# Performance work log

Hardware: AMD Instinct MI355X
Metric: run time of the kernel (lower is better)

Reference implementation:

```python
import jax, jax.numpy as jnp
import numpy as np

N = 50000          # nodes
E = 1_000_000      # edges
NODE_DIM = 16
EMB = 64           # embed_dim
OUT = 64           # out_dim per head
EA_DIM = 8         # raw edge_attr_dim
HEADS = 8
SLOPE = 0.01       # leaky_relu default negative slope
LN_EPS = 1e-5


def mlp(x, w, b, g, beta):
    # MLP(in, out): Linear -> LayerNorm -> ReLU (standard block in this repo)
    y = x @ w + b
    mu = jnp.mean(y, axis=-1, keepdims=True)
    var = jnp.var(y, axis=-1, keepdims=True)
    y = (y - mu) / jnp.sqrt(var + LN_EPS) * g + beta
    return jax.nn.relu(y)


def gat_layer(x, ea, src, tgt, W, a):
    """AA_GATlayer forward (dropout = identity at eval).
    x: [N, in], ea: [E, EMB], W: [in, OUT], a: [2*OUT + EMB]."""
    h = x @ W                                  # [N, OUT]
    d = h.shape[1]
    a_src, a_tgt, a_edge = a[:d], a[d:2 * d], a[2 * d:]
    # score = leaky_relu(a @ concat([h_src, h_tgt, ea])) without materializing the concat
    s = jax.nn.leaky_relu(h[src] @ a_src + h[tgt] @ a_tgt + ea @ a_edge, SLOPE)  # [E]
    s = s - jnp.max(s)
    e = jnp.exp(s)
    denom = jax.ops.segment_sum(e, src, num_segments=N)          # [N]
    attn = e / (denom[src] + 1e-16)                              # [E]
    h_prime = jax.ops.segment_sum(h[tgt] * attn[:, None], src, num_segments=N)  # [N, OUT]
    return jax.nn.elu(h_prime)


def setup_inputs() -> dict:
    key = jax.random.key(0)
    ks = jax.random.split(key, 16)
    sc = lambda fan_in: 1.0 / np.sqrt(fan_in)
    inp = {}
    inp["X"] = jax.random.normal(ks[0], (N, NODE_DIM), jnp.float32)
    inp["edge_attr"] = jax.random.normal(ks[1], (E, EA_DIM), jnp.float32)
    inp["edge_index"] = jax.random.randint(ks[2], (2, E), 0, N, jnp.int64)
    inp["matched_car_infra_nodes"] = jax.random.randint(ks[3], (1000,), 0, N, jnp.int64)
    # node_embed MLP params
    inp["w_node"] = jax.random.uniform(ks[4], (NODE_DIM, EMB), jnp.float32, -sc(NODE_DIM), sc(NODE_DIM))
    inp["b_node"] = jnp.zeros((EMB,), jnp.float32)
    inp["g_node"] = jnp.ones((EMB,), jnp.float32)
    inp["beta_node"] = jnp.zeros((EMB,), jnp.float32)
    # edge_attr_embed MLP params
    inp["w_edge"] = jax.random.uniform(ks[5], (EA_DIM, EMB), jnp.float32, -sc(EA_DIM), sc(EA_DIM))
    inp["b_edge"] = jnp.zeros((EMB,), jnp.float32)
    inp["g_edge"] = jnp.ones((EMB,), jnp.float32)
    inp["beta_edge"] = jnp.zeros((EMB,), jnp.float32)
    # 8 GAT heads: W [EMB,OUT], a [2*OUT+EMB]
    inp["gat_W"] = jax.random.uniform(ks[6], (HEADS, EMB, OUT), jnp.float32, -sc(EMB), sc(EMB))
    inp["gat_a"] = jax.random.uniform(ks[7], (HEADS, 2 * OUT + EMB), jnp.float32, -sc(2 * OUT + EMB), sc(2 * OUT + EMB))
    # output GAT layer: W [OUT*HEADS, OUT], a [2*OUT+EMB]
    inp["out_W"] = jax.random.uniform(ks[8], (OUT * HEADS, OUT), jnp.float32, -sc(OUT * HEADS), sc(OUT * HEADS))
    inp["out_a"] = jax.random.uniform(ks[9], (2 * OUT + EMB,), jnp.float32, -sc(2 * OUT + EMB), sc(2 * OUT + EMB))
    return inp


def reference(X, edge_attr, w_node, b_node, g_node, beta_node,
              w_edge, b_edge, g_edge, beta_edge,
              gat_W, gat_a, out_W, out_a,
              edge_index, matched_car_infra_nodes):
    src, tgt = edge_index[0], edge_index[1]
    x = mlp(X, w_node, b_node, g_node, beta_node)                  # [N, EMB]
    ea = mlp(edge_attr, w_edge, b_edge, g_edge, beta_edge)         # [E, EMB]
    heads = [gat_layer(x, ea, src, tgt, gat_W[i], gat_a[i]) for i in range(HEADS)]
    xh = jax.nn.elu(jnp.concatenate(heads, axis=1))                # [N, OUT*HEADS]
    out = gat_layer(xh, ea, src, tgt, out_W, out_a)                # [N, OUT]
    return jax.nn.log_softmax(out, axis=1)
```

## Files before the change

### kernel.cpp

```cpp
#include <hip/hip_runtime.h>
#include <hip/hip_fp16.h>

#define NN 50000
#define EE 1000000
#define HALF 25000

__device__ __forceinline__ float wsum(float v){
#pragma unroll
  for(int m=1;m<64;m<<=1) v += __shfl_xor(v,m,64);
  return v;
}
__device__ __forceinline__ unsigned encf(float f){
  unsigned u = __float_as_uint(f);
  return (u & 0x80000000u) ? ~u : (u | 0x80000000u);
}
__device__ __forceinline__ float decf(unsigned u){
  u = (u & 0x80000000u) ? (u & 0x7fffffffu) : ~u;
  return __uint_as_float(u);
}

__global__ __launch_bounds__(256) void zero_k(int* counts, int* cursor, unsigned* mx){
  int i = blockIdx.x*blockDim.x + threadIdx.x;
  if(i < NN){ counts[i] = 0; cursor[i] = 0; }
  if(i < 64) mx[i] = 0u;
}

__global__ __launch_bounds__(64) void cvec_k(const float* __restrict__ gat_W, const float* __restrict__ gat_a,
                                             float* __restrict__ cdir){
  int h = blockIdx.x, k = threadIdx.x;
  const float* W = gat_W + (size_t)h*64*64;
  const float* a = gat_a + (size_t)h*192;
  float cs = 0.f, ct = 0.f;
#pragma unroll
  for(int j=0;j<64;j++){ float wv = W[k*64+j]; cs += wv*a[j]; ct += wv*a[64+j]; }
  cdir[h*64 + k]       = cs;
  cdir[512 + h*64 + k] = ct;
}

__global__ __launch_bounds__(256) void node_mlp(const float* __restrict__ X, const float* __restrict__ w,
                                                const float* __restrict__ b, const float* __restrict__ g,
                                                const float* __restrict__ beta, const float* __restrict__ cdir,
                                                __half* __restrict__ x, float* __restrict__ ps8,
                                                float* __restrict__ pt8){
  int wid  = (blockIdx.x*blockDim.x + threadIdx.x) >> 6;
  int lane = threadIdx.x & 63;
  if(wid >= NN) return;
  float acc = b[lane];
#pragma unroll
  for(int k=0;k<16;k++) acc += X[wid*16+k] * w[k*64+lane];
  float mu  = wsum(acc) * (1.0f/64.0f);
  float d   = acc - mu;
  float var = wsum(d*d) * (1.0f/64.0f);
  float y   = d * rsqrtf(var + 1e-5f) * g[lane] + beta[lane];
  float xv  = fmaxf(y, 0.0f);
  x[(size_t)wid*64 + lane] = __float2half(xv);
#pragma unroll 1
  for(int h=0;h<8;h++){
    float a = wsum(xv * cdir[h*64+lane]);
    float c = wsum(xv * cdir[512 + h*64+lane]);
    if(lane == 0){ ps8[wid*8+h] = a; pt8[wid*8+h] = c; }
  }
}

__global__ __launch_bounds__(256) void hist_k(const int* __restrict__ src, int* __restrict__ counts){
  int e = blockIdx.x*blockDim.x + threadIdx.x;
  if(e < EE){
    int s = src[e];
    if((unsigned)s >= NN) s = 0;
    atomicAdd(&counts[s], 1);
  }
}

__global__ __launch_bounds__(256) void scan1_k(const int* __restrict__ counts, int* __restrict__ bsum){
  int i = blockIdx.x*256 + threadIdx.x;
  int v = (i < NN) ? counts[i] : 0;
  int s = v;
#pragma unroll
  for(int m=1;m<64;m<<=1) s += __shfl_xor(s,m,64);
  __shared__ int sm[4];
  if((threadIdx.x & 63) == 0) sm[threadIdx.x>>6] = s;
  __syncthreads();
  if(threadIdx.x == 0) bsum[blockIdx.x] = sm[0]+sm[1]+sm[2]+sm[3];
}

__global__ __launch_bounds__(256) void scan2_k(const int* __restrict__ bsum, int* __restrict__ bpre,
                                               int* __restrict__ offs){
  const int NB = (NN + 255)/256;
  int t = threadIdx.x;
  __shared__ int sm[256];
  int v = (t < NB) ? bsum[t] : 0;
  sm[t] = v; __syncthreads();
  for(int off=1; off<256; off<<=1){
    int u = (t >= off) ? sm[t-off] : 0;
    __syncthreads();
    sm[t] += u;
    __syncthreads();
  }
  if(t < NB) bpre[t] = sm[t] - v;
  if(t == 0) offs[NN] = EE;
}

__global__ __launch_bounds__(256) void scan3_k(const int* __restrict__ counts, const int* __restrict__ bpre,
                                               int* __restrict__ offs){
  int i = blockIdx.x*256 + threadIdx.x;
  int t = threadIdx.x;
  __shared__ int sm[256];
  int v = (i < NN) ? counts[i] : 0;
  sm[t] = v; __syncthreads();
  for(int off=1; off<256; off<<=1){
    int u = (t >= off) ? sm[t-off] : 0;
    __syncthreads();
    sm[t] += u;
    __syncthreads();
  }
  if(i < NN) offs[i] = bpre[blockIdx.x] + sm[t] - v;
}

__global__ __launch_bounds__(256) void scatter_k(const int* __restrict__ src, const int* __restrict__ tgt,
                                                 const int* __restrict__ offs, int* __restrict__ cursor,
                                                 int* __restrict__ rank, int* __restrict__ tgt_s,
                                                 int* __restrict__ src_s){
  int e = blockIdx.x*blockDim.x + threadIdx.x;
  if(e < EE){
    int s = src[e];
    if((unsigned)s >= NN) s = 0;
    int pos = offs[s] + atomicAdd(&cursor[s], 1);
    rank[e] = pos;
    int t = tgt[e];
    if((unsigned)t >= NN) t = 0;
    tgt_s[pos] = t;
    src_s[pos] = s;
  }
}

__global__ __launch_bounds__(256) void edge_mlp_q(const int* __restrict__ rank, const float* __restrict__ ea,
                                                  const float* __restrict__ w, const float* __restrict__ b,
                                                  const float* __restrict__ g, const float* __restrict__ beta,
                                                  const float* __restrict__ gat_a, const float* __restrict__ out_a,
                                                  float* __restrict__ q8, float* __restrict__ q_out){
  __shared__ float wle[512];
  __shared__ float ble[64], gle[64], bbe[64];
  __shared__ float ale[64*12];
  int tid = threadIdx.x;
  for(int idx=tid; idx<512; idx+=256){ int j=idx>>3, k=idx&7; wle[idx] = w[k*64+j]; }
  if(tid < 64){
    ble[tid] = b[tid]; gle[tid] = g[tid]; bbe[tid] = beta[tid];
#pragma unroll
    for(int r=0;r<8;r++) ale[tid*12+r] = gat_a[r*192 + 128 + tid];
    ale[tid*12+8] = out_a[128 + tid];
  }
  __syncthreads();
  int e = blockIdx.x*blockDim.x + tid;
  if(e >= EE) return;
  float4 ia = ((const float4*)ea)[(size_t)e*2];
  float4 ib = ((const float4*)ea)[(size_t)e*2+1];
  float y[64];
#pragma unroll
  for(int j=0;j<64;j++){
    float4 w0 = *(const float4*)&wle[j*8];
    float4 w1 = *(const float4*)&wle[j*8+4];
    float acc = ble[j];
    acc = fmaf(ia.x,w0.x, fmaf(ia.y,w0.y, fmaf(ia.z,w0.z, fmaf(ia.w,w0.w, acc))));
    acc = fmaf(ib.x,w1.x, fmaf(ib.y,w1.y, fmaf(ib.z,w1.z, fmaf(ib.w,w1.w, acc))));
    y[j] = acc;
  }
  float mu = 0.f;
#pragma unroll
  for(int j=0;j<64;j++) mu += y[j];
  mu *= (1.0f/64.0f);
  float var = 0.f;
#pragma unroll
  for(int j=0;j<64;j++){ float d = y[j]-mu; var += d*d; }
  var *= (1.0f/64.0f);
  float inv = rsqrtf(var + 1e-5f);
#pragma unroll
  for(int j=0;j<64;j++) y[j] = fmaxf((y[j]-mu)*inv*gle[j] + bbe[j], 0.0f);
  float qv[9];
#pragma unroll
  for(int r=0;r<9;r++) qv[r] = 0.f;
#pragma unroll
  for(int j=0;j<64;j++){
    float4 a0 = *(const float4*)&ale[j*12];
    float4 a1 = *(const float4*)&ale[j*12+4];
    float a8  = ale[j*12+8];
    float yj = y[j];
    qv[0]=fmaf(yj,a0.x,qv[0]); qv[1]=fmaf(yj,a0.y,qv[1]); qv[2]=fmaf(yj,a0.z,qv[2]); qv[3]=fmaf(yj,a0.w,qv[3]);
    qv[4]=fmaf(yj,a1.x,qv[4]); qv[5]=fmaf(yj,a1.y,qv[5]); qv[6]=fmaf(yj,a1.z,qv[6]); qv[7]=fmaf(yj,a1.w,qv[7]);
    qv[8]=fmaf(yj,a8 ,qv[8]);
  }
  int r = rank[e];
  ((float4*)q8)[(size_t)r*2]   = make_float4(qv[0],qv[1],qv[2],qv[3]);
  ((float4*)q8)[(size_t)r*2+1] = make_float4(qv[4],qv[5],qv[6],qv[7]);
  q_out[r] = qv[8];
}

__global__ __launch_bounds__(256) void maxq_k(const float* __restrict__ q8, const float* __restrict__ q_out,
                                              unsigned* __restrict__ mx){
  float m[9];
#pragma unroll
  for(int r=0;r<9;r++) m[r] = -3.0e38f;
  for(int i = blockIdx.x*256 + threadIdx.x; i < EE; i += gridDim.x*256){
    float4 a = ((const float4*)q8)[(size_t)i*2];
    float4 c = ((const float4*)q8)[(size_t)i*2+1];
    m[0]=fmaxf(m[0],a.x); m[1]=fmaxf(m[1],a.y); m[2]=fmaxf(m[2],a.z); m[3]=fmaxf(m[3],a.w);
    m[4]=fmaxf(m[4],c.x); m[5]=fmaxf(m[5],c.y); m[6]=fmaxf(m[6],c.z); m[7]=fmaxf(m[7],c.w);
    m[8]=fmaxf(m[8], q_out[i]);
  }
#pragma unroll
  for(int r=0;r<9;r++)
#pragma unroll
    for(int msk=1;msk<64;msk<<=1) m[r] = fmaxf(m[r], __shfl_xor(m[r],msk,64));
  __shared__ float sm[4][9];
  int wv = threadIdx.x>>6, lane = threadIdx.x&63;
  if(lane == 0){
#pragma unroll
    for(int r=0;r<9;r++) sm[wv][r] = m[r];
  }
  __syncthreads();
  if(threadIdx.x < 9){
    int r = threadIdx.x;
    float v = fmaxf(fmaxf(sm[0][r],sm[1][r]), fmaxf(sm[2][r],sm[3][r]));
    atomicMax(&mx[r], encf(v));
  }
}

__global__ __launch_bounds__(256) void maxp_k(const float* __restrict__ ps8, const float* __restrict__ pt8,
                                              unsigned* __restrict__ mx){
  float m[16];
#pragma unroll
  for(int r=0;r<16;r++) m[r] = -3.0e38f;
  for(int i = blockIdx.x*256 + threadIdx.x; i < NN; i += gridDim.x*256){
    float4 a = ((const float4*)ps8)[(size_t)i*2];
    float4 c = ((const float4*)ps8)[(size_t)i*2+1];
    float4 d = ((const float4*)pt8)[(size_t)i*2];
    float4 e = ((const float4*)pt8)[(size_t)i*2+1];
    m[0]=fmaxf(m[0],a.x); m[1]=fmaxf(m[1],a.y); m[2]=fmaxf(m[2],a.z); m[3]=fmaxf(m[3],a.w);
    m[4]=fmaxf(m[4],c.x); m[5]=fmaxf(m[5],c.y); m[6]=fmaxf(m[6],c.z); m[7]=fmaxf(m[7],c.w);
    m[8]=fmaxf(m[8],d.x); m[9]=fmaxf(m[9],d.y); m[10]=fmaxf(m[10],d.z); m[11]=fmaxf(m[11],d.w);
    m[12]=fmaxf(m[12],e.x); m[13]=fmaxf(m[13],e.y); m[14]=fmaxf(m[14],e.z); m[15]=fmaxf(m[15],e.w);
  }
#pragma unroll
  for(int r=0;r<16;r++)
#pragma unroll
    for(int msk=1;msk<64;msk<<=1) m[r] = fmaxf(m[r], __shfl_xor(m[r],msk,64));
  __shared__ float sm[4][16];
  int wv = threadIdx.x>>6, lane = threadIdx.x&63;
  if(lane == 0){
#pragma unroll
    for(int r=0;r<16;r++) sm[wv][r] = m[r];
  }
  __syncthreads();
  if(threadIdx.x < 16){
    int r = threadIdx.x;
    float v = fmaxf(fmaxf(sm[0][r],sm[1][r]), fmaxf(sm[2][r],sm[3][r]));
    atomicMax(&mx[16+r], encf(v));
  }
}

__global__ __launch_bounds__(256) void maxpo_k(const float* __restrict__ ps_o, const float* __restrict__ pt_o,
                                               unsigned* __restrict__ mx){
  float m0 = -3.0e38f, m1 = -3.0e38f;
  for(int i = blockIdx.x*256 + threadIdx.x; i < NN; i += gridDim.x*256){
    m0 = fmaxf(m0, ps_o[i]); m1 = fmaxf(m1, pt_o[i]);
  }
#pragma unroll
  for(int msk=1;msk<64;msk<<=1){ m0=fmaxf(m0,__shfl_xor(m0,msk,64)); m1=fmaxf(m1,__shfl_xor(m1,msk,64)); }
  __shared__ float sm[4][2];
  int wv = threadIdx.x>>6, lane = threadIdx.x&63;
  if(lane == 0){ sm[wv][0]=m0; sm[wv][1]=m1; }
  __syncthreads();
  if(threadIdx.x < 2){
    int r = threadIdx.x;
    float v = fmaxf(fmaxf(sm[0][r],sm[1][r]), fmaxf(sm[2][r],sm[3][r]));
    atomicMax(&mx[32+r], encf(v));
  }
}

__global__ __launch_bounds__(256) void score_k(const int* __restrict__ src_s, const int* __restrict__ tgt_s,
                                               const float* __restrict__ ps8, const float* __restrict__ pt8,
                                               const unsigned* __restrict__ mx, const float* __restrict__ q8,
                                               __half* __restrict__ w8h){
  int i = blockIdx.x*256 + threadIdx.x;
  if(i >= EE) return;
  int s = src_s[i], t = tgt_s[i];
  float4 qa = ((const float4*)q8)[(size_t)i*2];
  float4 qb = ((const float4*)q8)[(size_t)i*2+1];
  float4 sa = ((const float4*)ps8)[(size_t)s*2];
  float4 sb = ((const float4*)ps8)[(size_t)s*2+1];
  float4 ta = ((const float4*)pt8)[(size_t)t*2];
  float4 tb = ((const float4*)pt8)[(size_t)t*2+1];
  float sv[8] = {qa.x+sa.x+ta.x, qa.y+sa.y+ta.y, qa.z+sa.z+ta.z, qa.w+sa.w+ta.w,
                 qb.x+sb.x+tb.x, qb.y+sb.y+tb.y, qb.z+sb.z+tb.z, qb.w+sb.w+tb.w};
  float wv[8];
#pragma unroll
  for(int h=0;h<8;h++){
    float B = decf(mx[h]) + decf(mx[16+h]) + decf(mx[24+h]);
    float M = (B > 0.f) ? B : 0.01f*B;
    float x = sv[h];
    x = (x > 0.f) ? x : 0.01f*x;
    wv[h] = __expf(x - M);
  }
  __half2 p01 = __floats2half2_rn(wv[0],wv[1]);
  __half2 p23 = __floats2half2_rn(wv[2],wv[3]);
  __half2 p45 = __floats2half2_rn(wv[4],wv[5]);
  __half2 p67 = __floats2half2_rn(wv[6],wv[7]);
  uint4 pk;
  pk.x = *(unsigned*)&p01; pk.y = *(unsigned*)&p23;
  pk.z = *(unsigned*)&p45; pk.w = *(unsigned*)&p67;
  *(uint4*)(w8h + (size_t)i*8) = pk;
}

__global__ __launch_bounds__(256) void score_out_k(const int* __restrict__ src_s, const int* __restrict__ tgt_s,
                                                   const float* __restrict__ ps_o, const float* __restrict__ pt_o,
                                                   const unsigned* __restrict__ mx, float* __restrict__ q_out){
  int i = blockIdx.x*256 + threadIdx.x;
  if(i >= EE) return;
  float B = decf(mx[8]) + decf(mx[32]) + decf(mx[33]);
  float M = (B > 0.f) ? B : 0.01f*B;
  float x = ps_o[src_s[i]] + pt_o[tgt_s[i]] + q_out[i];
  x = (x > 0.f) ? x : 0.01f*x;
  q_out[i] = __expf(x - M);
}

__global__ __launch_bounds__(256) void agg_k(const int* __restrict__ offs, const int* __restrict__ tgt_s,
    const __half* __restrict__ w8h, const __half* __restrict__ x, __half* __restrict__ pre, int nbase){
  int wid  = nbase + ((blockIdx.x*blockDim.x + threadIdx.x) >> 6);
  int lane = threadIdx.x & 63;
  int quad = lane >> 4, l16 = lane & 15;
  int b  = offs[wid];
  int e2 = offs[wid+1];
  float  den[8];
  float4 num[8];
#pragma unroll
  for(int h=0;h<8;h++){ den[h] = 0.f; num[h] = make_float4(0.f,0.f,0.f,0.f); }
  for(int i=b+quad; i<e2; i+=4){
    int t = tgt_s[i];
    uint4 rw = *(const uint4*)(w8h + (size_t)i*8);
    float2 w01 = __half22float2(*(const __half2*)&rw.x);
    float2 w23 = __half22float2(*(const __half2*)&rw.y);
    float2 w45 = __half22float2(*(const __half2*)&rw.z);
    float2 w67 = __half22float2(*(const __half2*)&rw.w);
    uint2 raw = *(const uint2*)(x + (size_t)t*64 + l16*4);
    float2 fa = __half22float2(*(const __half2*)&raw.x);
    float2 fb = __half22float2(*(const __half2*)&raw.y);
    float4 xv = make_float4(fa.x, fa.y, fb.x, fb.y);
    float wv[8] = {w01.x,w01.y,w23.x,w23.y, w45.x,w45.y,w67.x,w67.y};
#pragma unroll
    for(int h=0;h<8;h++){
      den[h]   += wv[h];
      num[h].x = fmaf(wv[h],xv.x,num[h].x); num[h].y = fmaf(wv[h],xv.y,num[h].y);
      num[h].z = fmaf(wv[h],xv.z,num[h].z); num[h].w = fmaf(wv[h],xv.w,num[h].w);
    }
  }
#pragma unroll
  for(int h=0;h<8;h++){
    den[h]   += __shfl_xor(den[h],16,64);   den[h]   += __shfl_xor(den[h],32,64);
    num[h].x += __shfl_xor(num[h].x,16,64); num[h].x += __shfl_xor(num[h].x,32,64);
    num[h].y += __shfl_xor(num[h].y,16,64); num[h].y += __shfl_xor(num[h].y,32,64);
    num[h].z += __shfl_xor(num[h].z,16,64); num[h].z += __shfl_xor(num[h].z,32,64);
    num[h].w += __shfl_xor(num[h].w,16,64); num[h].w += __shfl_xor(num[h].w,32,64);
  }
  __half* dst = pre + (size_t)(wid - nbase)*512;
#pragma unroll
  for(int k=0;k<2;k++){
    int h = 2*quad + k;
    float invd = (den[h] > 0.f) ? 1.0f/den[h] : 0.f;
    __half2 h0 = __floats2half2_rn(num[h].x*invd, num[h].y*invd);
    __half2 h1 = __floats2half2_rn(num[h].z*invd, num[h].w*invd);
    uint2 pk; pk.x = *(unsigned*)&h0; pk.y = *(unsigned*)&h1;
    *(uint2*)(dst + h*64 + l16*4) = pk;
  }
}

__global__ __launch_bounds__(256) void transform_k(const __half* __restrict__ pre,
                                                   const float* __restrict__ gat_W,
                                                   const float* __restrict__ outW,
                                                   float* __restrict__ h2p,
                                                   int nbase, int cn){
  __shared__ float pz[64*68];
  __shared__ float Wl[4096];
  __shared__ float Ol[4096];
  int tid = threadIdx.x;
  int n0  = blockIdx.x * 64;
  int g   = blockIdx.y;
  h2p += (size_t)g * NN * 64;
  int a   = tid >> 4;
  int b   = tid & 15;
  float outacc[16];
#pragma unroll
  for(int i=0;i<16;i++) outacc[i] = 0.f;
#pragma unroll 1
  for(int hh=0; hh<4; hh++){
    int h = g*4 + hh;
    __syncthreads();
    const float4* Wg = (const float4*)(gat_W + (size_t)h*4096);
    const float4* Og = (const float4*)(outW  + (size_t)h*4096);
#pragma unroll
    for(int r4=0;r4<4;r4++){
      int f4 = r4*256 + tid;
      ((float4*)Wl)[f4] = Wg[f4];
      ((float4*)Ol)[f4] = Og[f4];
    }
#pragma unroll
    for(int r4=0;r4<4;r4++){
      int idx = r4*256 + tid;
      int n = idx >> 4, j4 = idx & 15;
      int gn = n0 + n;
      uint2 raw = make_uint2(0u, 0u);
      if(gn < cn) raw = *(const uint2*)(pre + (size_t)gn*512 + h*64 + j4*4);
      float2 fa = __half22float2(*(const __half2*)&raw.x);
      float2 fb = __half22float2(*(const __half2*)&raw.y);
      pz[(j4*4+0)*68 + n] = fa.x;
      pz[(j4*4+1)*68 + n] = fa.y;
      pz[(j4*4+2)*68 + n] = fb.x;
      pz[(j4*4+3)*68 + n] = fb.y;
    }
    __syncthreads();
    float v[16];
#pragma unroll
    for(int i=0;i<16;i++) v[i] = 0.f;
#pragma unroll 4
    for(int j=0;j<64;j++){
      float4 pn = *(const float4*)&pz[j*68 + a*4];
      float4 wc = *(const float4*)&Wl[j*64 + b*4];
#pragma unroll
      for(int na=0;na<4;na++){
        float pv = (&pn.x)[na];
        v[na*4+0] = fmaf(pv, wc.x, v[na*4+0]);
        v[na*4+1] = fmaf(pv, wc.y, v[na*4+1]);
        v[na*4+2] = fmaf(pv, wc.z, v[na*4+2]);
        v[na*4+3] = fmaf(pv, wc.w, v[na*4+3]);
      }
    }
    __syncthreads();
#pragma unroll
    for(int cb=0;cb<4;cb++){
      float4 z4;
#pragma unroll
      for(int na=0;na<4;na++){
        float z  = (v[na*4+cb] > 0.f) ? v[na*4+cb] : expm1f(v[na*4+cb]);
        float z2 = (z > 0.f) ? z : expm1f(z);
        (&z4.x)[na] = z2;
      }
      *(float4*)&pz[(b*4+cb)*68 + a*4] = z4;
    }
    __syncthreads();
#pragma unroll 4
    for(int c=0;c<64;c++){
      float4 zn = *(const float4*)&pz[c*68 + a*4];
      float4 oc = *(const float4*)&Ol[c*64 + b*4];
#pragma unroll
      for(int na=0;na<4;na++){
        float zv = (&zn.x)[na];
        outacc[na*4+0] = fmaf(zv, oc.x, outacc[na*4+0]);
        outacc[na*4+1] = fmaf(zv, oc.y, outacc[na*4+1]);
        outacc[na*4+2] = fmaf(zv, oc.z, outacc[na*4+2]);
        outacc[na*4+3] = fmaf(zv, oc.w, outacc[na*4+3]);
      }
    }
  }
#pragma unroll
  for(int na=0;na<4;na++){
    int nl = n0 + a*4 + na;
    if(nl < cn){
      float4 o = make_float4(outacc[na*4+0], outacc[na*4+1], outacc[na*4+2], outacc[na*4+3]);
      *(float4*)&h2p[(size_t)(nbase + nl)*64 + b*4] = o;
    }
  }
}

__global__ __launch_bounds__(256) void finalize_po(const float* __restrict__ p0, const float* __restrict__ p1,
                                                   const float* __restrict__ out_a, __half* __restrict__ h2f,
                                                   float* __restrict__ ps_o, float* __restrict__ pt_o){
  int wid  = (blockIdx.x*blockDim.x + threadIdx.x) >> 6;
  int lane = threadIdx.x & 63;
  if(wid >= NN) return;
  float v = p0[(size_t)wid*64 + lane] + p1[(size_t)wid*64 + lane];
  float ps = wsum(v * out_a[lane]);
  float pt = wsum(v * out_a[64+lane]);
  if(lane == 0){ ps_o[wid] = ps; pt_o[wid] = pt; }
  h2f[(size_t)wid*64 + lane] = __float2half(v);
}

__global__ __launch_bounds__(256) void agg_out(const int* __restrict__ offs, const int* __restrict__ tgt_s,
                                               const float* __restrict__ w_out, const __half* __restrict__ h2f,
                                               float* __restrict__ dout){
  int wid  = (blockIdx.x*blockDim.x + threadIdx.x) >> 6;
  int lane = threadIdx.x & 63;
  if(wid >= NN) return;
  int quad = lane >> 4, l16 = lane & 15;
  int b  = offs[wid];
  int e2 = offs[wid+1];
  float4 num = make_float4(0.f,0.f,0.f,0.f);
  float den = 0.f;
  for(int i=b+quad; i<e2; i+=4){
    int t = tgt_s[i];
    float w = w_out[i];
    uint2 raw = *(const uint2*)(h2f + (size_t)t*64 + l16*4);
    float2 fa = __half22float2(*(const __half2*)&raw.x);
    float2 fb = __half22float2(*(const __half2*)&raw.y);
    den += w;
    num.x = fmaf(w,fa.x,num.x); num.y = fmaf(w,fa.y,num.y);
    num.z = fmaf(w,fb.x,num.z); num.w = fmaf(w,fb.y,num.w);
  }
  den   += __shfl_xor(den,16,64);   den   += __shfl_xor(den,32,64);
  num.x += __shfl_xor(num.x,16,64); num.x += __shfl_xor(num.x,32,64);
  num.y += __shfl_xor(num.y,16,64); num.y += __shfl_xor(num.y,32,64);
  num.z += __shfl_xor(num.z,16,64); num.z += __shfl_xor(num.z,32,64);
  num.w += __shfl_xor(num.w,16,64); num.w += __shfl_xor(num.w,32,64);
  float inv = (den > 0.f) ? 1.0f/den : 0.f;
  float z[4];
  float mloc = -3.0e38f;
#pragma unroll
  for(int k=0;k<4;k++){
    float hp = ((&num.x)[k]) * inv;
    z[k] = (hp > 0.f) ? hp : expm1f(hp);
    mloc = fmaxf(mloc, z[k]);
  }
#pragma unroll
  for(int msk=1; msk<16; msk<<=1) mloc = fmaxf(mloc, __shfl_xor(mloc,msk,64));
  float ssum = 0.f;
#pragma unroll
  for(int k=0;k<4;k++) ssum += __expf(z[k] - mloc);
#pragma unroll
  for(int msk=1; msk<16; msk<<=1) ssum += __shfl_xor(ssum,msk,64);
  float lse = mloc + logf(ssum);
  if(quad == 0){
    float4 o = make_float4(z[0]-lse, z[1]-lse, z[2]-lse, z[3]-lse);
    ((float4*)dout)[(size_t)wid*16 + l16] = o;
  }
}

extern "C" void kernel_launch(void* const* d_in, const int* in_sizes, int n_in,
                              void* d_out, int out_size, void* d_ws, size_t ws_size,
                              hipStream_t stream) {
  const float* X         = (const float*)d_in[0];
  const float* edge_attr = (const float*)d_in[1];
  const int*   edge_index= (const int*)d_in[2];
  const float* w_node    = (const float*)d_in[4];
  const float* b_node    = (const float*)d_in[5];
  const float* g_node    = (const float*)d_in[6];
  const float* beta_node = (const float*)d_in[7];
  const float* w_edge    = (const float*)d_in[8];
  const float* b_edge    = (const float*)d_in[9];
  const float* g_edge    = (const float*)d_in[10];
  const float* beta_edge = (const float*)d_in[11];
  const float* gat_W     = (const float*)d_in[12];
  const float* gat_a     = (const float*)d_in[13];
  const float* out_W     = (const float*)d_in[14];
  const float* out_a     = (const float*)d_in[15];
  float* dout = (float*)d_out;

  const int* src = edge_index;
  const int* tgt = edge_index + EE;

  char* base = (char*)d_ws;
  size_t off = 0;
  auto take = [&](size_t bytes)->char*{ char* p = base + off; off += (bytes + 31) & ~(size_t)31; return p; };
  int*      counts = (int*)     take((size_t)NN*4);
  int*      cursor = (int*)     take((size_t)NN*4);
  int*      offs   = (int*)     take((size_t)(NN+1)*4);
  int*      bsum   = (int*)     take(256*4);
  int*      bpre   = (int*)     take(256*4);
  unsigned* mx     = (unsigned*)take(64*4);
  float*    ps_o   = (float*)   take((size_t)NN*4);
  float*    pt_o   = (float*)   take((size_t)NN*4);
  float*    cdir   = (float*)   take(1024*4);
  int*      rank   = (int*)     take((size_t)EE*4);
  int*      tgt_s  = (int*)     take((size_t)EE*4);
  int*      src_s  = (int*)     take((size_t)EE*4);
  float*    ps8    = (float*)   take((size_t)NN*8*4);
  float*    pt8    = (float*)   take((size_t)NN*8*4);
  __half*   xh     = (__half*)  take((size_t)NN*64*2);
  __half*   h2fh   = (__half*)  take((size_t)NN*64*2);
  float*    h2p    = (float*)   take((size_t)2*NN*64*4);
  float*    q8     = (float*)   take((size_t)EE*8*4);
  __half*   w8h    = (__half*)  take((size_t)EE*8*2);
  float*    q_out  = (float*)   take((size_t)EE*4);
  __half*   pre    = (__half*)  take((size_t)HALF*512*2);

  const int NBLK_N  = (NN*64 + 255)/256;
  const int NBLK_E  = (EE + 255)/256;
  const int NBLK_S  = (NN + 255)/256;
  const int NBLK_A  = HALF/4;
  const int NBLK_T  = (HALF + 63)/64;

  zero_k   <<<NBLK_S, 256, 0, stream>>>(counts, cursor, mx);
  cvec_k   <<<8,       64, 0, stream>>>(gat_W, gat_a, cdir);
  node_mlp <<<NBLK_N, 256, 0, stream>>>(X, w_node, b_node, g_node, beta_node, cdir, xh, ps8, pt8);
  hist_k   <<<NBLK_E, 256, 0, stream>>>(src, counts);
  scan1_k  <<<NBLK_S, 256, 0, stream>>>(counts, bsum);
  scan2_k  <<<1,      256, 0, stream>>>(bsum, bpre, offs);
  scan3_k  <<<NBLK_S, 256, 0, stream>>>(counts, bpre, offs);
  scatter_k<<<NBLK_E, 256, 0, stream>>>(src, tgt, offs, cursor, rank, tgt_s, src_s);
  edge_mlp_q<<<NBLK_E,256, 0, stream>>>(rank, edge_attr, w_edge, b_edge, g_edge, beta_edge,
                                        gat_a, out_a, q8, q_out);
  maxq_k   <<<1024,   256, 0, stream>>>(q8, q_out, mx);
  maxp_k   <<<128,    256, 0, stream>>>(ps8, pt8, mx);
  score_k  <<<NBLK_E, 256, 0, stream>>>(src_s, tgt_s, ps8, pt8, mx, q8, w8h);

  for(int half=0; half<2; half++){
    int nbase = half*HALF;
    agg_k<<<NBLK_A, 256, 0, stream>>>(offs, tgt_s, w8h, xh, pre, nbase);
    dim3 tg((unsigned)NBLK_T, 2);
    transform_k<<<tg, 256, 0, stream>>>(pre, gat_W, out_W, h2p, nbase, HALF);
  }

  finalize_po<<<NBLK_N, 256, 0, stream>>>(h2p, h2p + (size_t)NN*64, out_a, h2fh, ps_o, pt_o);
  maxpo_k    <<<128,  256, 0, stream>>>(ps_o, pt_o, mx);
  score_out_k<<<NBLK_E,256, 0, stream>>>(src_s, tgt_s, ps_o, pt_o, mx, q_out);
  agg_out    <<<NBLK_N,256, 0, stream>>>(offs, tgt_s, q_out, h2fh, dout);
}
```

Baseline: 757.9 us.

## Use fp16 MFMA for per-head transform and output projection

Replaces the scalar FP32 shared-memory GEMM in the transform kernel with MFMA 16x16x32 fp16 instructions. Per-head W and out_W are pre-converted to transposed fp16 by a new small kernel. The ELU intermediate is staged through a swizzled per-wave LDS tile instead of block-wide syncs. This cuts FMA instruction count and barriers, but drops the intermediate z and the weights to fp16 precision.

```diff
diff --git a/kernel.cpp b/kernel.cpp
--- a/kernel.cpp
+++ b/kernel.cpp
@@ -4,6 +4,9 @@
 #define NN 50000
 #define EE 1000000
 #define HALF 25000
+
+typedef _Float16 h8v __attribute__((ext_vector_type(8)));
+typedef float    f4a __attribute__((ext_vector_type(4)));
 
 __device__ __forceinline__ float wsum(float v){
 #pragma unroll
@@ -35,6 +38,16 @@
   for(int j=0;j<64;j++){ float wv = W[k*64+j]; cs += wv*a[j]; ct += wv*a[64+j]; }
   cdir[h*64 + k]       = cs;
   cdir[512 + h*64 + k] = ct;
+}
+
+__global__ __launch_bounds__(256) void cvtw_k(const float* __restrict__ gat_W, const float* __restrict__ out_W,
+                                              __half* __restrict__ WT, __half* __restrict__ OT){
+  int h = blockIdx.x; int tid = threadIdx.x;
+  for(int idx = tid; idx < 4096; idx += 256){
+    int j = idx >> 6, k = idx & 63;
+    WT[(size_t)h*4096 + k*64 + j] = __float2half(gat_W[(size_t)h*4096 + j*64 + k]);
+    OT[(size_t)h*4096 + k*64 + j] = __float2half(out_W[(size_t)h*4096 + j*64 + k]);
+  }
 }
 
 __global__ __launch_bounds__(256) void node_mlp(const float* __restrict__ X, const float* __restrict__ w,
@@ -372,99 +385,71 @@
   }
 }
 
-__global__ __launch_bounds__(256) void transform_k(const __half* __restrict__ pre,
-                                                   const float* __restrict__ gat_W,
-                                                   const float* __restrict__ outW,
-                                                   float* __restrict__ h2p,
-                                                   int nbase, int cn){
-  __shared__ float pz[64*68];
-  __shared__ float Wl[4096];
-  __shared__ float Ol[4096];
+__global__ __launch_bounds__(256) void transform_mfma(const __half* __restrict__ pre,
+                                                      const __half* __restrict__ WT,
+                                                      const __half* __restrict__ OT,
+                                                      float* __restrict__ h2p,
+                                                      int nbase, int cn){
+  __shared__ __half zl[4*16*64];
   int tid = threadIdx.x;
-  int n0  = blockIdx.x * 64;
-  int g   = blockIdx.y;
+  int w  = tid >> 6, l = tid & 63;
+  int lr = l & 15, lg = l >> 4;
+  int n0 = blockIdx.x * 64;
+  int g  = blockIdx.y;
   h2p += (size_t)g * NN * 64;
-  int a   = tid >> 4;
-  int b   = tid & 15;
-  float outacc[16];
-#pragma unroll
-  for(int i=0;i<16;i++) outacc[i] = 0.f;
+  int gn  = n0 + w*16 + lr;
+  int gnr = (gn < cn) ? gn : 0;
+  __half* zw = zl + w*1024;
+  f4a out[4];
+#pragma unroll
+  for(int i=0;i<4;i++){ out[i][0]=0.f; out[i][1]=0.f; out[i][2]=0.f; out[i][3]=0.f; }
 #pragma unroll 1
   for(int hh=0; hh<4; hh++){
     int h = g*4 + hh;
-    __syncthreads();
-    const float4* Wg = (const float4*)(gat_W + (size_t)h*4096);
-    const float4* Og = (const float4*)(outW  + (size_t)h*4096);
-#pragma unroll
-    for(int r4=0;r4<4;r4++){
-      int f4 = r4*256 + tid;
-      ((float4*)Wl)[f4] = Wg[f4];
-      ((float4*)Ol)[f4] = Og[f4];
+    h8v a1_0 = *(const h8v*)(pre + (size_t)gnr*512 + h*64 + 0*32 + lg*8);
+    h8v a1_1 = *(const h8v*)(pre + (size_t)gnr*512 + h*64 + 1*32 + lg*8);
+    f4a zacc[4];
+#pragma unroll
+    for(int nt=0; nt<4; nt++){ zacc[nt][0]=0.f; zacc[nt][1]=0.f; zacc[nt][2]=0.f; zacc[nt][3]=0.f; }
+    const __half* WTh = WT + (size_t)h*4096;
+#pragma unroll
+    for(int nt=0; nt<4; nt++){
+      h8v b0 = *(const h8v*)(WTh + (nt*16 + lr)*64 + 0*32 + lg*8);
+      h8v b1 = *(const h8v*)(WTh + (nt*16 + lr)*64 + 1*32 + lg*8);
+      zacc[nt] = __builtin_amdgcn_mfma_f32_16x16x32_f16(a1_0, b0, zacc[nt], 0, 0, 0);
+      zacc[nt] = __builtin_amdgcn_mfma_f32_16x16x32_f16(a1_1, b1, zacc[nt], 0, 0, 0);
     }
 #pragma unroll
-    for(int r4=0;r4<4;r4++){
-      int idx = r4*256 + tid;
-      int n = idx >> 4, j4 = idx & 15;
-      int gn = n0 + n;
-      uint2 raw = make_uint2(0u, 0u);
-      if(gn < cn) raw = *(const uint2*)(pre + (size_t)gn*512 + h*64 + j4*4);
-      float2 fa = __half22float2(*(const __half2*)&raw.x);
-      float2 fb = __half22float2(*(const __half2*)&raw.y);
-      pz[(j4*4+0)*68 + n] = fa.x;
-      pz[(j4*4+1)*68 + n] = fa.y;
-      pz[(j4*4+2)*68 + n] = fb.x;
-      pz[(j4*4+3)*68 + n] = fb.y;
-    }
-    __syncthreads();
-    float v[16];
-#pragma unroll
-    for(int i=0;i<16;i++) v[i] = 0.f;
-#pragma unroll 4
-    for(int j=0;j<64;j++){
-      float4 pn = *(const float4*)&pz[j*68 + a*4];
-      float4 wc = *(const float4*)&Wl[j*64 + b*4];
-#pragma unroll
-      for(int na=0;na<4;na++){
-        float pv = (&pn.x)[na];
-        v[na*4+0] = fmaf(pv, wc.x, v[na*4+0]);
-        v[na*4+1] = fmaf(pv, wc.y, v[na*4+1]);
-        v[na*4+2] = fmaf(pv, wc.z, v[na*4+2]);
-        v[na*4+3] = fmaf(pv, wc.w, v[na*4+3]);
+    for(int nt=0; nt<4; nt++){
+#pragma unroll
+      for(int r=0; r<4; r++){
+        float v = zacc[nt][r];
+        float z = (v > 0.f) ? v : expm1f(v);
+        z = (z > 0.f) ? z : expm1f(z);
+        int rho = lg*4 + r;
+        int c   = nt*16 + lr;
+        int pc  = (((c>>3) ^ (rho&7))<<3) | (c&7);
+        zw[rho*64 + pc] = __float2half(z);
       }
     }
-    __syncthreads();
-#pragma unroll
-    for(int cb=0;cb<4;cb++){
-      float4 z4;
-#pragma unroll
-      for(int na=0;na<4;na++){
-        float z  = (v[na*4+cb] > 0.f) ? v[na*4+cb] : expm1f(v[na*4+cb]);
-        float z2 = (z > 0.f) ? z : expm1f(z);
-        (&z4.x)[na] = z2;
-      }
-      *(float4*)&pz[(b*4+cb)*68 + a*4] = z4;
-    }
-    __syncthreads();
-#pragma unroll 4
-    for(int c=0;c<64;c++){
-      float4 zn = *(const float4*)&pz[c*68 + a*4];
-      float4 oc = *(const float4*)&Ol[c*64 + b*4];
-#pragma unroll
-      for(int na=0;na<4;na++){
-        float zv = (&zn.x)[na];
-        outacc[na*4+0] = fmaf(zv, oc.x, outacc[na*4+0]);
-        outacc[na*4+1] = fmaf(zv, oc.y, outacc[na*4+1]);
-        outacc[na*4+2] = fmaf(zv, oc.z, outacc[na*4+2]);
-        outacc[na*4+3] = fmaf(zv, oc.w, outacc[na*4+3]);
+    const __half* OTh = OT + (size_t)h*4096;
+#pragma unroll
+    for(int ks=0; ks<2; ks++){
+      int Gp = (lg + 4*ks) ^ (lr & 7);
+      h8v a2 = *(const h8v*)(zw + lr*64 + Gp*8);
+#pragma unroll
+      for(int nt=0; nt<4; nt++){
+        h8v b2 = *(const h8v*)(OTh + (nt*16 + lr)*64 + ks*32 + lg*8);
+        out[nt] = __builtin_amdgcn_mfma_f32_16x16x32_f16(a2, b2, out[nt], 0, 0, 0);
       }
     }
   }
 #pragma unroll
-  for(int na=0;na<4;na++){
-    int nl = n0 + a*4 + na;
-    if(nl < cn){
-      float4 o = make_float4(outacc[na*4+0], outacc[na*4+1], outacc[na*4+2], outacc[na*4+3]);
-      *(float4*)&h2p[(size_t)(nbase + nl)*64 + b*4] = o;
+  for(int nt=0; nt<4; nt++){
+#pragma unroll
+    for(int r=0; r<4; r++){
+      int grow = n0 + w*16 + lg*4 + r;
+      if(grow < cn) h2p[(size_t)(nbase + grow)*64 + nt*16 + lr] = out[nt][r];
     }
   }
 }
@@ -573,6 +558,8 @@
   float*    pt8    = (float*)   take((size_t)NN*8*4);
   __half*   xh     = (__half*)  take((size_t)NN*64*2);
   __half*   h2fh   = (__half*)  take((size_t)NN*64*2);
+  __half*   WT16   = (__half*)  take((size_t)8*4096*2);
+  __half*   OT16   = (__half*)  take((size_t)8*4096*2);
   float*    h2p    = (float*)   take((size_t)2*NN*64*4);
   float*    q8     = (float*)   take((size_t)EE*8*4);
   __half*   w8h    = (__half*)  take((size_t)EE*8*2);
@@ -587,6 +574,7 @@
 
   zero_k   <<<NBLK_S, 256, 0, stream>>>(counts, cursor, mx);
   cvec_k   <<<8,       64, 0, stream>>>(gat_W, gat_a, cdir);
+  cvtw_k   <<<8,      256, 0, stream>>>(gat_W, out_W, WT16, OT16);
   node_mlp <<<NBLK_N, 256, 0, stream>>>(X, w_node, b_node, g_node, beta_node, cdir, xh, ps8, pt8);
   hist_k   <<<NBLK_E, 256, 0, stream>>>(src, counts);
   scan1_k  <<<NBLK_S, 256, 0, stream>>>(counts, bsum);
@@ -603,7 +591,7 @@
     int nbase = half*HALF;
     agg_k<<<NBLK_A, 256, 0, stream>>>(offs, tgt_s, w8h, xh, pre, nbase);
     dim3 tg((unsigned)NBLK_T, 2);
-    transform_k<<<tg, 256, 0, stream>>>(pre, gat_W, out_W, h2p, nbase, HALF);
+    transform_mfma<<<tg, 256, 0, stream>>>(pre, WT16, OT16, h2p, nbase, HALF);
   }
 
   finalize_po<<<NBLK_N, 256, 0, stream>>>(h2p, h2p + (size_t)NN*64, out_a, h2fh, ps_o, pt_o);
```

After: 685.9 us. 9.5% less time.
